# Optimization experiments

Hardware: AMD Instinct MI355X
Metric: run time of the kernel (lower is better)

The kernel has to match this reference:

```python
import jax, jax.numpy as jnp
import numpy as np

SCALING = 2.5
OFFSET = 0.0
TIME_LENGTH = 10.0
DT = 0.1
CUTOFF = TIME_LENGTH  # cutoff=None -> time_length
TIME_STEPS = int(TIME_LENGTH // DT) + 1  # == 100 (float floor: 10.0//0.1 == 99.0)
CENTERS = np.array([-1.75, -1.25, -0.75, -0.25, 0.25, 0.75, 1.25, 1.75], dtype=np.float32)


def setup_inputs() -> dict:
    key = jax.random.key(0)
    k1, = jax.random.split(key, 1)
    trace = jax.random.normal(k1, (1024, 128), dtype=jnp.float32)
    center = jnp.asarray(CENTERS)
    return {"trace": trace, "center": center, "dummy1": 0, "dummy2": 0}


def reference(trace, center, dummy1, dummy2):
    B = trace.shape[0]
    # times: [B, F*C] latency per (feature, center) pair
    times = SCALING * jnp.abs(trace[..., None] - center).reshape(B, -1)
    times = jnp.where((times < 0) | (times > CUTOFF), TIME_LENGTH + DT, times)
    times = times + OFFSET
    bins = (times / DT + 1).astype(jnp.int32)  # trunc == floor for positive values
    mask = bins < TIME_STEPS
    N = times.shape[1]
    bi = jnp.broadcast_to(jnp.arange(B)[:, None], (B, N))
    ni = jnp.broadcast_to(jnp.arange(N)[None, :], (B, N))
    bins_c = jnp.clip(bins, 0, TIME_STEPS - 1)
    vals = mask.astype(jnp.int32)
    # masked scatter-add into pre-zeroed dense spike tensor (COO to_dense sums dups)
    spikes = jnp.zeros((TIME_STEPS, B, N), dtype=jnp.int32).at[bins_c, bi, ni].add(vals)
    return spikes
```

## Files before the change

kernel.cpp:

```cpp
#include <hip/hip_runtime.h>
#include <hip/hip_bf16.h>


#define BB 1024
#define FF 128
#define NN 1024
#define TT 100
#define GROUPS_PER_PLANE ((BB * NN) / 4)
#define NGROUPS (TT * GROUPS_PER_PLANE)
#define P2_BLOCKS 4096
#define P2_THREADS 256
#define P2_ITERS (NGROUPS / (P2_BLOCKS * P2_THREADS))

typedef int iv4 __attribute__((ext_vector_type(4)));

__global__ __launch_bounds__(256) void arnold_bins_kernel(
        const float* __restrict__ trace,
        const float* __restrict__ center,
        uchar4* __restrict__ bins) {
    const int b   = blockIdx.x;
    const int tid = threadIdx.x;
    const int n0  = tid << 2;
    const int f   = n0 >> 3;
    const int c0  = n0 & 7;

    const float x = trace[b * FF + f];

    unsigned char v[4];
#pragma unroll
    for (int i = 0; i < 4; ++i) {
        float tms = 2.5f * fabsf(x - center[c0 + i]);
        unsigned bb = (tms > 10.0f) ? 255u : (unsigned)(tms / 0.1f + 1.0f);
        v[i] = (unsigned char)bb;
    }
    bins[(b << 8) + tid] = make_uchar4(v[0], v[1], v[2], v[3]);
}

__global__ __launch_bounds__(256) void arnold_stream_kernel(
        const uchar4* __restrict__ bins,
        iv4* __restrict__ out) {
    const int base = blockIdx.x * (P2_ITERS * P2_THREADS) + threadIdx.x;
#pragma unroll
    for (int k = 0; k < P2_ITERS; ++k) {
        const int g = base + k * P2_THREADS;
        const int t = g >> 18;
        const int p = g & (GROUPS_PER_PLANE - 1);
        const uchar4 c = bins[p];
        iv4 v;
        v.x = (c.x == t) ? 1 : 0;
        v.y = (c.y == t) ? 1 : 0;
        v.z = (c.z == t) ? 1 : 0;
        v.w = (c.w == t) ? 1 : 0;
        __builtin_nontemporal_store(v, &out[g]);
    }
}

extern "C" void kernel_launch(void* const* d_in, const int* in_sizes, int n_in,
                              void* d_out, int out_size, void* d_ws, size_t ws_size,
                              hipStream_t stream) {
    const float* trace  = (const float*)d_in[0];
    const float* center = (const float*)d_in[1];
    uchar4* bins = (uchar4*)d_ws;
    iv4* out = (iv4*)d_out;

    arnold_bins_kernel<<<BB, 256, 0, stream>>>(trace, center, bins);
    arnold_stream_kernel<<<P2_BLOCKS, P2_THREADS, 0, stream>>>(bins, out);
}
```

Before: 419.9 us.

## Stage bin windows in shared memory and reuse across time-step chunks

The streaming kernel now loads a 2048-entry window of precomputed bins into LDS once per block and writes ten time planes from it, on a 2D grid of windows by time chunks. Before, every output group re-read its bin byte from global memory, so bin reads were repeated once per time step. This trades those redundant global reads for LDS traffic and a barrier, and changes the write pattern to strided plane writes per block.

```diff
diff --git a/kernel.cpp b/kernel.cpp
--- a/kernel.cpp
+++ b/kernel.cpp
@@ -7,10 +7,10 @@
 #define NN 1024
 #define TT 100
 #define GROUPS_PER_PLANE ((BB * NN) / 4)
-#define NGROUPS (TT * GROUPS_PER_PLANE)
-#define P2_BLOCKS 4096
-#define P2_THREADS 256
-#define P2_ITERS (NGROUPS / (P2_BLOCKS * P2_THREADS))
+#define WINDOW 2048
+#define WINS (GROUPS_PER_PLANE / WINDOW)
+#define PCH 10
+#define PCHUNKS (TT / PCH)
 
 typedef int iv4 __attribute__((ext_vector_type(4)));
 
@@ -39,19 +39,32 @@
 __global__ __launch_bounds__(256) void arnold_stream_kernel(
         const uchar4* __restrict__ bins,
         iv4* __restrict__ out) {
-    const int base = blockIdx.x * (P2_ITERS * P2_THREADS) + threadIdx.x;
+    __shared__ uchar4 lb[WINDOW];
+    const int w   = blockIdx.x;
+    const int pc  = blockIdx.y;
+    const int tid = threadIdx.x;
+
+    const uchar4* bw = bins + w * WINDOW;
 #pragma unroll
-    for (int k = 0; k < P2_ITERS; ++k) {
-        const int g = base + k * P2_THREADS;
-        const int t = g >> 18;
-        const int p = g & (GROUPS_PER_PLANE - 1);
-        const uchar4 c = bins[p];
-        iv4 v;
-        v.x = (c.x == t) ? 1 : 0;
-        v.y = (c.y == t) ? 1 : 0;
-        v.z = (c.z == t) ? 1 : 0;
-        v.w = (c.w == t) ? 1 : 0;
-        __builtin_nontemporal_store(v, &out[g]);
+    for (int i = 0; i < WINDOW / 256; ++i) lb[i * 256 + tid] = bw[i * 256 + tid];
+    __syncthreads();
+
+    const int t0 = pc * PCH;
+    iv4* base = out + (size_t)w * WINDOW;
+    for (int tt = 0; tt < PCH; ++tt) {
+        const int t = t0 + tt;
+        iv4* op = base + (size_t)t * GROUPS_PER_PLANE;
+#pragma unroll
+        for (int i = 0; i < WINDOW / 256; ++i) {
+            const int idx = i * 256 + tid;
+            const uchar4 c = lb[idx];
+            iv4 v;
+            v.x = (c.x == t) ? 1 : 0;
+            v.y = (c.y == t) ? 1 : 0;
+            v.z = (c.z == t) ? 1 : 0;
+            v.w = (c.w == t) ? 1 : 0;
+            __builtin_nontemporal_store(v, &op[idx]);
+        }
     }
 }
 
@@ -64,5 +77,6 @@
     iv4* out = (iv4*)d_out;
 
     arnold_bins_kernel<<<BB, 256, 0, stream>>>(trace, center, bins);
-    arnold_stream_kernel<<<P2_BLOCKS, P2_THREADS, 0, stream>>>(bins, out);
+    dim3 grid(WINS, PCHUNKS);
+    arnold_stream_kernel<<<grid, 256, 0, stream>>>(bins, out);
 }
```

After: 416.5 us. No clear change (-0.8%).
